# Performance work log

Hardware: AMD Instinct MI355X
Metric: run time of the kernel (lower is better)

## Reference

```python
import jax, jax.numpy as jnp
import numpy as np

L, B, S, H, NH, HD = 2, 2, 1024, 768, 12, 64
E, K, F, V = 8, 2, 3072, 50257
THETA = 10000.0
EPS = 1e-5


def setup_inputs() -> dict:
    key = jax.random.key(0)
    ks = iter(jax.random.split(key, 40))
    def nrm(shape):
        return jax.random.normal(next(ks), shape, jnp.float32) * 0.02
    return {
        "input_ids": jax.random.randint(next(ks), (B, S), 0, V),
        "emb": nrm((V, H)),
        "ln1_w": jnp.ones((L, H)), "ln1_b": jnp.zeros((L, H)),
        "ln2_w": jnp.ones((L, H)), "ln2_b": jnp.zeros((L, H)),
        "lnf_w": jnp.ones((H,)), "lnf_b": jnp.zeros((H,)),
        "Wq": nrm((L, H, H)), "bq": jnp.zeros((L, H)),
        "Wk": nrm((L, H, H)), "bk": jnp.zeros((L, H)),
        "Wv": nrm((L, H, H)), "bv": jnp.zeros((L, H)),
        "Wo": nrm((L, H, H)), "bo": jnp.zeros((L, H)),
        "Wr": nrm((L, H, E)), "br": jnp.zeros((L, E)),
        "W1": nrm((L, E, H, F)), "b1": jnp.zeros((L, E, F)),
        "W2": nrm((L, E, F, H)), "b2": jnp.zeros((L, E, H)),
    }


def _layer_norm(x, w, b):
    m = x.mean(-1, keepdims=True)
    v = ((x - m) ** 2).mean(-1, keepdims=True)
    return (x - m) * jax.lax.rsqrt(v + EPS) * w + b


def _rotate_half(x):
    x1, x2 = jnp.split(x, 2, axis=-1)
    return jnp.concatenate([-x2, x1], axis=-1)


def _forward(input_ids, emb, ln1_w, ln1_b, ln2_w, ln2_b, lnf_w, lnf_b,
             Wq, bq, Wk, bk, Wv, bv, Wo, bo, Wr, br, W1, b1, W2, b2):
    x = emb[input_ids]  # [B,S,H]

    # RoPE tables [1,1,S,HD]
    inv_freq = 1.0 / (THETA ** (jnp.arange(0, HD, 2, dtype=jnp.float32) / HD))
    freqs = jnp.arange(S, dtype=jnp.float32)[:, None] * inv_freq[None, :]
    ang = jnp.concatenate([freqs, freqs], axis=-1)
    cos = jnp.cos(ang)[None, None].astype(x.dtype)
    sin = jnp.sin(ang)[None, None].astype(x.dtype)

    causal = jnp.where(jnp.tril(jnp.ones((S, S), dtype=bool)), 0.0, -1e9)
    causal = causal[None, None].astype(x.dtype)

    scale = 1.0 / np.sqrt(HD)
    for l in range(L):
        # --- attention block ---
        h = _layer_norm(x, ln1_w[l], ln1_b[l])
        q = (h @ Wq[l] + bq[l]).reshape(B, S, NH, HD).transpose(0, 2, 1, 3)
        k = (h @ Wk[l] + bk[l]).reshape(B, S, NH, HD).transpose(0, 2, 1, 3)
        v = (h @ Wv[l] + bv[l]).reshape(B, S, NH, HD).transpose(0, 2, 1, 3)
        q = q * cos + _rotate_half(q) * sin
        k = k * cos + _rotate_half(k) * sin
        scores = jnp.einsum('bhqd,bhkd->bhqk', q, k) * scale + causal
        attn = jax.nn.softmax(scores, axis=-1)
        o = jnp.einsum('bhqk,bhkd->bhqd', attn, v)
        o = o.transpose(0, 2, 1, 3).reshape(B, S, H)
        x = x + (o @ Wo[l] + bo[l])

        # --- MoE feed-forward block ---
        h = _layer_norm(x, ln2_w[l], ln2_b[l]).reshape(-1, H)  # [N,H]
        router_probs = jax.nn.softmax(h @ Wr[l] + br[l], axis=-1)  # [N,E]
        tp, ti = jax.lax.top_k(router_probs, K)
        tp = tp / (tp.sum(-1, keepdims=True) + 1e-9)
        # combine weights per expert (equiv. to the per-slot scatter loop)
        w = (jax.nn.one_hot(ti, E, dtype=h.dtype) * tp[..., None]).sum(1)  # [N,E]
        a = jax.nn.gelu(jnp.einsum('nh,ehf->nef', h, W1[l]) + b1[l], approximate=False)
        oe = jnp.einsum('nef,efh->neh', a, W2[l]) + b2[l]
        ff = jnp.einsum('ne,neh->nh', w, oe)
        x = x + ff.reshape(B, S, H)

    x = _layer_norm(x, lnf_w, lnf_b)
    logits = jnp.einsum('bsh,vh->bsv', x, emb)  # tied lm_head
    return logits


def reference(input_ids, emb, ln1_w, ln1_b, ln2_w, ln2_b, lnf_w, lnf_b,
              Wq, bq, Wk, bk, Wv, bv, Wo, bo, Wr, br, W1, b1, W2, b2):
    return _forward(input_ids, emb, ln1_w, ln1_b, ln2_w, ln2_b, lnf_w, lnf_b,
                    Wq, bq, Wk, bk, Wv, bv, Wo, bo, Wr, br, W1, b1, W2, b2)
```

## Files before the change

kernel.cpp:

```cpp
#include <hip/hip_runtime.h>
#include <stdint.h>

constexpr int L = 2, Bb = 2, S = 1024, H = 768, NHd = 12, HD = 64;
constexpr int E = 8, F = 3072, V = 50257;
constexpr int NTOK = Bb * S;
constexpr int NSLOT = NTOK * 2;
constexpr float EPSLN = 1e-5f;

typedef __attribute__((ext_vector_type(4))) float f32x4;
typedef __attribute__((ext_vector_type(8))) short s16x8;

#define DEVI __device__ __forceinline__

DEVI float bf2f(short u) {
  union { float f; uint32_t i; } c; c.i = ((uint32_t)(uint16_t)u) << 16; return c.f;
}
DEVI short f2bf(float f) {
  union { float f; uint32_t i; } c; c.f = f;
  uint32_t x = c.i;
  uint32_t r = (x + 0x7fffu + ((x >> 16) & 1u)) >> 16;
  return (short)r;
}

DEVI void gload16(const void* g, void* l) {
  __builtin_amdgcn_global_load_lds(g, l, 16, 0, 0);
}

DEVI float gelu1(float g) { return 0.5f * g * (1.f + erff(g * 0.70710678118f)); }

__global__ void k_f32_to_bf16(const float* __restrict__ in, short* __restrict__ out, long n4) {
  long i = (long)blockIdx.x * blockDim.x + threadIdx.x;
  if (i >= n4) return;
  long base = i * 4;
  f32x4 v = *(const f32x4*)(in + base);
  short4 o;
  o.x = f2bf(v.x); o.y = f2bf(v.y); o.z = f2bf(v.z); o.w = f2bf(v.w);
  *(short4*)(out + base) = o;
}

__global__ void k_split(const float* __restrict__ in, short* __restrict__ oh,
                        short* __restrict__ ol, long n4) {
  long i = (long)blockIdx.x * blockDim.x + threadIdx.x;
  if (i >= n4) return;
  long base = i * 4;
  f32x4 v = *(const f32x4*)(in + base);
  short4 h, l;
  h.x = f2bf(v.x); l.x = f2bf(v.x - bf2f(h.x));
  h.y = f2bf(v.y); l.y = f2bf(v.y - bf2f(h.y));
  h.z = f2bf(v.z); l.z = f2bf(v.z - bf2f(h.z));
  h.w = f2bf(v.w); l.w = f2bf(v.w - bf2f(h.w));
  *(short4*)(oh + base) = h;
  *(short4*)(ol + base) = l;
}

__global__ void k_split3(const float* __restrict__ in, short* __restrict__ o0,
                         short* __restrict__ o1, short* __restrict__ o2, long n4) {
  long i = (long)blockIdx.x * blockDim.x + threadIdx.x;
  if (i >= n4) return;
  long base = i * 4;
  f32x4 v = *(const f32x4*)(in + base);
  short4 a, b, c;
#define SP3(comp)                                    \
  {                                                  \
    float x = v.comp;                                \
    short t0 = f2bf(x);                              \
    float r = x - bf2f(t0);                          \
    short t1 = f2bf(r);                              \
    short t2 = f2bf(r - bf2f(t1));                   \
    a.comp = t0; b.comp = t1; c.comp = t2;           \
  }
  SP3(x) SP3(y) SP3(z) SP3(w)
#undef SP3
  *(short4*)(o0 + base) = a;
  *(short4*)(o1 + base) = b;
  *(short4*)(o2 + base) = c;
}

__global__ void k_transpose_bf16(const float* __restrict__ in, short* __restrict__ out,
                                 int R, int C, long inBS, long outBS) {
  __shared__ float tile[32][33];
  const float* src = in + (size_t)blockIdx.z * inBS;
  short* dst = out + (size_t)blockIdx.z * outBS;
  int r0 = blockIdx.y * 32, c0 = blockIdx.x * 32;
  int tx = threadIdx.x, ty = threadIdx.y;
#pragma unroll
  for (int i = 0; i < 32; i += 8) {
    int r = r0 + ty + i, c = c0 + tx;
    if (r < R && c < C) tile[ty + i][tx] = src[(size_t)r * C + c];
  }
  __syncthreads();
#pragma unroll
  for (int i = 0; i < 32; i += 8) {
    int c = c0 + ty + i, r = r0 + tx;
    if (r < R && c < C) dst[(size_t)c * R + r] = f2bf(tile[tx][ty + i]);
  }
}

__global__ void k_transpose_split(const float* __restrict__ in, short* __restrict__ oh,
                                  short* __restrict__ ol, int R, int C, long inBS,
                                  long outBS) {
  __shared__ float tile[32][33];
  const float* src = in + (size_t)blockIdx.z * inBS;
  short* dh = oh + (size_t)blockIdx.z * outBS;
  short* dl = ol + (size_t)blockIdx.z * outBS;
  int r0 = blockIdx.y * 32, c0 = blockIdx.x * 32;
  int tx = threadIdx.x, ty = threadIdx.y;
#pragma unroll
  for (int i = 0; i < 32; i += 8) {
// ... 12 lines not shown
      dl[(size_t)c * R + r] = lo;
    }
  }
}

__global__ void k_transpose_split3(const float* __restrict__ in, short* __restrict__ o0,
                                   short* __restrict__ o1, short* __restrict__ o2,
                                   int R, int C) {
  __shared__ float tile[32][33];
  int r0 = blockIdx.y * 32, c0 = blockIdx.x * 32;
  int tx = threadIdx.x, ty = threadIdx.y;
#pragma unroll
  for (int i = 0; i < 32; i += 8) {
    int r = r0 + ty + i, c = c0 + tx;
    if (r < R && c < C) tile[ty + i][tx] = in[(size_t)r * C + c];
  }
  __syncthreads();
#pragma unroll
  for (int i = 0; i < 32; i += 8) {
    int c = c0 + ty + i, r = r0 + tx;
    if (r < R && c < C) {
      float v = tile[tx][ty + i];
      short t0 = f2bf(v);
      float rr = v - bf2f(t0);
      short t1 = f2bf(rr);
      short t2 = f2bf(rr - bf2f(t1));
      o0[(size_t)c * R + r] = t0;
      o1[(size_t)c * R + r] = t1;
      o2[(size_t)c * R + r] = t2;
    }
  }
}

__global__ void k_bqkv(const float* __restrict__ bq, const float* __restrict__ bk,
                       const float* __restrict__ bv, float* __restrict__ bqkv) {
  int i = blockIdx.x * blockDim.x + threadIdx.x;
  if (i >= L * 3 * H) return;
  int l = i / (3 * H), j = i % (3 * H);
  float v = (j < H) ? bq[l * H + j] : (j < 2 * H) ? bk[l * H + j - H] : bv[l * H + j - 2 * H];
  bqkv[i] = v;
}

__global__ void k_ropetab(float* __restrict__ cosT, float* __restrict__ sinT) {
  int i = blockIdx.x * blockDim.x + threadIdx.x;
  if (i >= S * (HD / 2)) return;
  int s = i / 32, d = i % 32;
  float invf = powf(10000.f, -(2.f * d) / (float)HD);
  float ang = (float)s * invf;
  cosT[i] = cosf(ang);
  sinT[i] = sinf(ang);
}

__global__ void k_embed(const int* __restrict__ ids, const float* __restrict__ emb,
                        float* __restrict__ x) {
  int idx = blockIdx.x * blockDim.x + threadIdx.x;
  int row = idx / (H / 4), c4 = idx % (H / 4);
  if (row >= NTOK) return;
  int t = ids[row];
  ((f32x4*)(x + (size_t)row * H))[c4] = ((const f32x4*)(emb + (size_t)t * H))[c4];
}

template <bool BF>
__global__ void k_layernorm(const float* __restrict__ x, const float* __restrict__ w,
                            const float* __restrict__ b, void* __restrict__ outp) {
  int row = blockIdx.x * (blockDim.x >> 6) + (threadIdx.x >> 6);
  int lane = threadIdx.x & 63;
  if (row >= NTOK) return;
  const float* xr = x + (size_t)row * H;
  float v[12], s = 0.f, s2 = 0.f;
#pragma unroll
  for (int j = 0; j < 12; j++) { float t = xr[lane + j * 64]; v[j] = t; s += t; s2 += t * t; }
#pragma unroll
  for (int off = 32; off; off >>= 1) { s += __shfl_xor(s, off); s2 += __shfl_xor(s2, off); }
  float m = s / (float)H;
  float var = s2 / (float)H - m * m;
  float rs = 1.f / sqrtf(var + EPSLN);
#pragma unroll
  for (int j = 0; j < 12; j++) {
    int c = lane + j * 64;
    float val = (v[j] - m) * rs * w[c] + b[c];
    if (BF) ((short*)outp)[(size_t)row * H + c] = f2bf(val);
    else    ((float*)outp)[(size_t)row * H + c] = val;
  }
}

__global__ void k_rope(const float* __restrict__ qkv, const float* __restrict__ bqkv,
                       const float* __restrict__ cosT, const float* __restrict__ sinT,
                       float* __restrict__ qf, float* __restrict__ kf,
                       float* __restrict__ vT) {
  int idx = blockIdx.x * blockDim.x + threadIdx.x;
  if (idx >= Bb * S * NHd * 32) return;
  int d = idx & 31;
  int h = (idx >> 5) % NHd;
  int t = idx / (32 * NHd);
  int s = t % S, b = t / S;
  const float* base = qkv + (size_t)t * (3 * H) + h * HD;
  const float* bb = bqkv + h * HD;
  float c = cosT[s * 32 + d], sn = sinT[s * 32 + d];
  float q1 = base[d] + bb[d],               q2 = base[d + 32] + bb[d + 32];
  float k1 = base[H + d] + bb[H + d],       k2 = base[H + d + 32] + bb[H + d + 32];
  float v1 = base[2 * H + d] + bb[2 * H + d], v2 = base[2 * H + d + 32] + bb[2 * H + d + 32];
  size_t z = (size_t)(b * NHd + h);
  size_t qk = (z * S + s) * HD;
  qf[qk + d]      = q1 * c - q2 * sn;
  qf[qk + d + 32] = q2 * c + q1 * sn;
  kf[qk + d]      = k1 * c - k2 * sn;
  kf[qk + d + 32] = k2 * c + k1 * sn;
  size_t vb = z * HD * S + s;
  vT[vb + (size_t)d * S]        = v1;
  vT[vb + (size_t)(d + 32) * S] = v2;
}

__global__ void k_softmax2(short* __restrict__ p0, short* __restrict__ p1) {
  int row = blockIdx.x * 4 + (threadIdx.x >> 6);
  int lane = threadIdx.x & 63;
  s16x8* r0 = (s16x8*)(p0 + (size_t)row * S + lane * 16);
  s16x8* r1 = (s16x8*)(p1 + (size_t)row * S + lane * 16);
  s16x8 h0 = r0[0], h1 = r0[1];
  s16x8 l0 = r1[0], l1 = r1[1];
  float v[16];
#pragma unroll
  for (int j = 0; j < 8; j++) {
    v[j] = bf2f(h0[j]) + bf2f(l0[j]);
    v[8 + j] = bf2f(h1[j]) + bf2f(l1[j]);
  }
  float mx = -3e38f;
#pragma unroll
  for (int j = 0; j < 16; j++) mx = fmaxf(mx, v[j]);
#pragma unroll
  for (int off = 32; off; off >>= 1) mx = fmaxf(mx, __shfl_xor(mx, off));
  float sum = 0.f;
#pragma unroll
  for (int j = 0; j < 16; j++) { v[j] = expf(v[j] - mx); sum += v[j]; }
#pragma unroll
  for (int off = 32; off; off >>= 1) sum += __shfl_xor(sum, off);
  float inv = 1.f / sum;
#pragma unroll
  for (int j = 0; j < 16; j++) v[j] *= inv;
  s16x8 oh0, oh1, ol0, ol1;
#pragma unroll
  for (int j = 0; j < 8; j++) {
    short hi = f2bf(v[j]);
    oh0[j] = hi; ol0[j] = f2bf(v[j] - bf2f(hi));
// ... 63 lines not shown
  if (tok >= NTOK) return;
  for (int k = 0; k < 2; k++) {
    int e = sel_e[tok * 2 + k];
    int pos = atomicAdd(cursor + e, 1);
    int g = offs[e] + pos;
    tok_list[g] = tok;
    slot_of[tok * 2 + k] = g;
  }
}

__global__ void k_combine(const float* __restrict__ oe, const float* __restrict__ sel_w,
                          const int* __restrict__ slot_of, const int* __restrict__ sel_e,
                          const float* __restrict__ b2, float* __restrict__ x) {
  int idx = blockIdx.x * blockDim.x + threadIdx.x;
  if (idx >= NTOK * (H / 4)) return;
  int tok = idx / (H / 4), c4 = idx % (H / 4);
  float w0 = sel_w[tok * 2], w1 = sel_w[tok * 2 + 1];
  int s0 = slot_of[tok * 2], s1 = slot_of[tok * 2 + 1];
  int e0 = sel_e[tok * 2], e1 = sel_e[tok * 2 + 1];
  f32x4 a = ((const f32x4*)(oe + (size_t)s0 * H))[c4];
  f32x4 b = ((const f32x4*)(oe + (size_t)s1 * H))[c4];
  f32x4 ba = ((const f32x4*)(b2 + (size_t)e0 * H))[c4];
  f32x4 bb = ((const f32x4*)(b2 + (size_t)e1 * H))[c4];
  f32x4* xp = (f32x4*)(x + (size_t)tok * H) + c4;
  *xp = *xp + w0 * (a + ba) + w1 * (b + bb);
}

template <int SP, int MODE, bool GATHER>
__global__ __launch_bounds__(256, 2) void k_bgemmS(
    const short* __restrict__ A0, const short* __restrict__ A1, const short* __restrict__ A2,
    long sAz, int lda,
    const short* __restrict__ B0, const short* __restrict__ B1, const short* __restrict__ B2,
    long sBz, int ldb,
    void* __restrict__ Cp, void* __restrict__ Cp2, int zdiv, long sChi, long sClo, int ldc,
    const float* __restrict__ res, const float* __restrict__ bias, long sBias,
    int M, int N, int K,
    const int* __restrict__ d_counts, const int* __restrict__ d_offs,
    const int* __restrict__ gidx, float alpha) {
  const int z = blockIdx.z;
  const int Meff = d_counts ? d_counts[z] : M;
  const int tm = blockIdx.y;
  if (tm * 128 >= Meff) return;
  const int tn = blockIdx.x;
  const int row_base = d_offs ? d_offs[z] : 0;

  __shared__ short Ab[SP][128 * 32];
  __shared__ short Bb2[SP][128 * 32];

  const int tid = threadIdx.x;
  const int lane = tid & 63;
  const int w = tid >> 6;

  const short* APz[3];
  const short* BPz[3];
  APz[0] = A0 + (size_t)z * sAz;
  APz[1] = A1 + (size_t)z * sAz;
  APz[2] = (SP > 2) ? (A2 + (size_t)z * sAz) : APz[0];
  BPz[0] = B0 + (size_t)z * sBz;
  BPz[1] = B1 + (size_t)z * sBz;
  BPz[2] = (SP > 2) ? (B2 + (size_t)z * sBz) : BPz[0];

  size_t aOff[2], bOff[2];
#pragma unroll
  for (int i = 0; i < 2; ++i) {
    const int srow = i * 64 + (tid >> 2);
    const int kb = (tid & 3) ^ (srow & 3);
    int lrow = tm * 128 + srow;
// ... 27 lines not shown
  for (int k0 = 0; k0 < K; k0 += 32) {
#pragma unroll
    for (int s = 0; s < SP; ++s) {
      gload16(APz[s] + aOff[0], (char*)(&Ab[s][0]) + w * 1024);
      gload16(APz[s] + aOff[1], (char*)(&Ab[s][0]) + 4096 + w * 1024);
      gload16(BPz[s] + bOff[0], (char*)(&Bb2[s][0]) + w * 1024);
      gload16(BPz[s] + bOff[1], (char*)(&Bb2[s][0]) + 4096 + w * 1024);
    }
    aOff[0] += 32; aOff[1] += 32; bOff[0] += 32; bOff[1] += 32;
    __syncthreads();
    s16x8 af[SP][4], bf[SP][4];
#pragma unroll
    for (int s = 0; s < SP; ++s)
#pragma unroll
      for (int i = 0; i < 4; ++i) {
        af[s][i] = *(const s16x8*)(&Ab[s][aoff[i]]);
        bf[s][i] = *(const s16x8*)(&Bb2[s][boff[i]]);
      }
#pragma unroll
    for (int mi = 0; mi < 4; ++mi)
#pragma unroll
      for (int ni = 0; ni < 4; ++ni) {
        f32x4 a = acc[mi][ni];
#pragma unroll
        for (int si = 0; si < SP; ++si)
#pragma unroll
          for (int sj = 0; sj < SP - si; ++sj)
            a = __builtin_amdgcn_mfma_f32_16x16x32_bf16(af[si][mi], bf[sj][ni], a, 0, 0, 0);
        acc[mi][ni] = a;
      }
    __syncthreads();
  }

  const long out_off = (long)(z / zdiv) * sChi + (long)(z % zdiv) * sClo;
  const float* bz = bias ? (bias + (size_t)z * sBias) : nullptr;
  const int q4 = lane >> 4;
  float bvv[4];
  int gco[4];
#pragma unroll
  for (int ni = 0; ni < 4; ++ni) {
    gco[ni] = tn * 128 + wc + ni * 16 + r16;
    bvv[ni] = (bz && gco[ni] < N) ? bz[gco[ni]] : 0.f;
  }
#pragma unroll
  for (int mi = 0; mi < 4; ++mi) {
#pragma unroll
    for (int j = 0; j < 4; ++j) {
      const int lrow = tm * 128 + wr + mi * 16 + q4 * 4 + j;
      if (lrow >= Meff) continue;
      const long rbase = out_off + (long)(row_base + lrow) * ldc;
#pragma unroll
      for (int ni = 0; ni < 4; ++ni) {
        if (gco[ni] >= N) continue;
        const float v = acc[mi][ni][j];
        const long idx = rbase + gco[ni];
        if (MODE == 0) {
          ((float*)Cp)[idx] = v + bvv[ni];
        } else if (MODE == 1) {
          ((float*)Cp)[idx] = res[idx] + v + bvv[ni];
        } else if (MODE == 6) {
          float g = gelu1(v + bvv[ni]);
          short hi = f2bf(g);
          ((short*)Cp)[idx] = hi;
          ((short*)Cp2)[idx] = f2bf(g - bf2f(hi));
        } else if (MODE == 7) {
          float g = v * alpha + ((gco[ni] > lrow) ? -1e9f : 0.f);
          short hi = f2bf(g);
          ((short*)Cp)[idx] = hi;
          ((short*)Cp2)[idx] = f2bf(g - bf2f(hi));
        }
      }
    }
  }
}

template <int SP, int MODE, bool GATHER>
static void bgemmS(hipStream_t st, const short* A0, const short* A1, const short* A2, long sAz,
                   int lda, const short* B0, const short* B1, const short* B2, long sBz,
                   int ldb, void* C, void* C2, int zdiv, long sChi, long sClo, int ldc,
                   const float* res, const float* bias, long sBias, int M, int N, int K,
                   int nz, const int* cnts, const int* offs_, const int* gat, float alpha) {
  dim3 g((N + 127) / 128, (M + 127) / 128, nz);
  k_bgemmS<SP, MODE, GATHER><<<g, 256, 0, st>>>(A0, A1, A2, sAz, lda, B0, B1, B2, sBz, ldb, C,
                                                C2, zdiv, sChi, sClo, ldc, res, bias, sBias, M,
                                                N, K, cnts, offs_, gat, alpha);
}

template <int MODE, bool GATHER, bool NSWZ>
__global__ __launch_bounds__(256, 2) void k_bgemm(
    const short* __restrict__ A, long sAz, int lda,
    const short* __restrict__ Bt, long sBz, int ldb,
    void* __restrict__ Cp, int zdiv, long sChi, long sClo, int ldc,
    const float* __restrict__ bias, long sBias,
    int M, int N, int K,
    const int* __restrict__ d_counts, const int* __restrict__ d_offs,
    const int* __restrict__ gidx) {
  const int z = blockIdx.z;
  const int Meff = d_counts ? d_counts[z] : M;
  int tm, tn;
  if (NSWZ) {
    const int bid = blockIdx.y * gridDim.x + blockIdx.x;
    const int nwg = gridDim.x * gridDim.y;
    const int q = nwg >> 3, r = nwg & 7;
    const int xcd = bid & 7, ix = bid >> 3;
    const int wg = (xcd < r) ? (xcd * (q + 1) + ix) : (r * (q + 1) + (xcd - r) * q + ix);
    tn = wg / gridDim.y;
    tm = wg % gridDim.y;
  } else {
    tm = blockIdx.y;
    tn = blockIdx.x;
  }
  if (tm * 128 >= Meff) return;
  const int row_base = d_offs ? d_offs[z] : 0;

  __shared__ short Abuf[128 * 32];
  __shared__ short Bbuf[128 * 32];

  const int tid = threadIdx.x;
  const int lane = tid & 63;
  const int w = tid >> 6;

  const short* Az = A + (size_t)z * sAz;
  const short* Bz = Bt + (size_t)z * sBz;

  const short* aSrc[2];
  const short* bSrc[2];
#pragma unroll
  for (int i = 0; i < 2; ++i) {
    const int srow = i * 64 + (tid >> 2);
    const int kb = (tid & 3) ^ (srow & 3);
    int lrow = tm * 128 + srow;
    if (lrow > Meff - 1) lrow = Meff - 1;
    int ar = row_base + lrow;
    if (GATHER) ar = gidx[ar];
    aSrc[i] = Az + (size_t)ar * lda + kb * 8;
    int bcol = tn * 128 + srow;
    if (bcol > N - 1) bcol = N - 1;
    bSrc[i] = Bz + (size_t)bcol * ldb + kb * 8;
  }

  f32x4 acc[4][4];
#pragma unroll
  for (int a = 0; a < 4; ++a)
#pragma unroll
    for (int b = 0; b < 4; ++b) acc[a][b] = {0.f, 0.f, 0.f, 0.f};

  const int wr = (w >> 1) * 64;
  const int wc = (w & 1) * 64;
  const int r16 = lane & 15;
  const int kb4 = lane >> 4;
  const int swz = (kb4 ^ (r16 & 3)) * 8;
  int aoff[4], boff[4];
#pragma unroll
  for (int i = 0; i < 4; ++i) {
    aoff[i] = (wr + i * 16 + r16) * 32 + swz;
    boff[i] = (wc + i * 16 + r16) * 32 + swz;
  }
  char* const ldsA0 = (char*)Abuf + w * 1024;
  char* const ldsA1 = (char*)Abuf + 4096 + w * 1024;
  char* const ldsB0 = (char*)Bbuf + w * 1024;
  char* const ldsB1 = (char*)Bbuf + 4096 + w * 1024;

  for (int k0 = 0; k0 < K; k0 += 32) {
    gload16(aSrc[0], ldsA0);
    gload16(aSrc[1], ldsA1);
    gload16(bSrc[0], ldsB0);
    gload16(bSrc[1], ldsB1);
    aSrc[0] += 32; aSrc[1] += 32; bSrc[0] += 32; bSrc[1] += 32;
    __syncthreads();
    s16x8 af[4], bf[4];
#pragma unroll
    for (int i = 0; i < 4; ++i) {
      af[i] = *(const s16x8*)(Abuf + aoff[i]);
      bf[i] = *(const s16x8*)(Bbuf + boff[i]);
    }
#pragma unroll
    for (int mi = 0; mi < 4; ++mi)
#pragma unroll
      for (int ni = 0; ni < 4; ++ni)
        acc[mi][ni] =
            __builtin_amdgcn_mfma_f32_16x16x32_bf16(af[mi], bf[ni], acc[mi][ni], 0, 0, 0);
    __syncthreads();
  }

  const long out_off = (long)(z / zdiv) * sChi + (long)(z % zdiv) * sClo;
  const float* bz = bias ? (bias + (size_t)z * sBias) : nullptr;
  const int q4 = lane >> 4;
  float bvv[4];
  int gco[4];
#pragma unroll
  for (int ni = 0; ni < 4; ++ni) {
    gco[ni] = tn * 128 + wc + ni * 16 + r16;
    bvv[ni] = (bz && gco[ni] < N) ? bz[gco[ni]] : 0.f;
  }
#pragma unroll
  for (int mi = 0; mi < 4; ++mi) {
#pragma unroll
    for (int j = 0; j < 4; ++j) {
      const int lrow = tm * 128 + wr + mi * 16 + q4 * 4 + j;
      if (lrow >= Meff) continue;
      const long rbase = out_off + (row_base + lrow) * (long)ldc;
#pragma unroll
      for (int ni = 0; ni < 4; ++ni) {
        if (gco[ni] >= N) continue;
        const float v = acc[mi][ni][j];
        if (MODE == 0) {
          ((float*)Cp)[rbase + gco[ni]] = v + bvv[ni];
        } else if (MODE == 4) {
          float g = v + bvv[ni];
          ((short*)Cp)[rbase + gco[ni]] = f2bf(gelu1(g));
        }
      }
    }
  }
// ... 30 lines not shown
  const float* Wo = (const float*)d_in[14];
  const float* bo = (const float*)d_in[15];
  const float* Wr = (const float*)d_in[16];
  const float* br = (const float*)d_in[17];
  const float* W1 = (const float*)d_in[18];
  const float* b1 = (const float*)d_in[19];
  const float* W2 = (const float*)d_in[20];
  const float* b2 = (const float*)d_in[21];
  float* out = (float*)d_out;

  char* p = (char*)d_ws;
  auto alloc = [&](size_t bytes) {
    char* r = p;
    p += (bytes + 255) & ~(size_t)255;
    return r;
  };
  short* embB = (short*)alloc((size_t)V * H * 2);
  char* big = alloc((size_t)Bb * NHd * S * S * 2 * 2);
  short* p0   = (short*)big;
  short* p1   = p0 + (size_t)Bb * NHd * S * S;
  short* R_hi = (short*)big;
  short* R_lo = R_hi + (size_t)E * F * H;
  short* Wb0 = (short*)alloc((size_t)3 * H * H * 2);
  short* Wb1 = (short*)alloc((size_t)3 * H * H * 2);
  short* Wb2 = (short*)alloc((size_t)3 * H * H * 2);
  short* Wo0 = (short*)alloc((size_t)H * H * 2);
  short* Wo1 = (short*)alloc((size_t)H * H * 2);
  short* Wo2 = (short*)alloc((size_t)H * H * 2);
  float* bqkv = (float*)alloc((size_t)L * 3 * H * 4);
  float* cosT = (float*)alloc((size_t)S * 32 * 4);
  float* sinT = (float*)alloc((size_t)S * 32 * 4);
  float* x    = (float*)alloc((size_t)NTOK * H * 4);
  float* hbuf = (float*)alloc((size_t)NTOK * H * 4);
  float* qf   = (float*)alloc((size_t)NTOK * H * 4);
  float* kf   = (float*)alloc((size_t)NTOK * H * 4);
  float* vT   = (float*)alloc((size_t)NTOK * H * 4);
  float* o    = (float*)alloc((size_t)NTOK * H * 4);
  short* xb   = (short*)alloc((size_t)NTOK * H * 2);
  short* xb2  = (short*)alloc((size_t)NTOK * H * 2);
  short* h_hi = (short*)alloc((size_t)NTOK * H * 2);
  short* h_lo = (short*)alloc((size_t)NTOK * H * 2);
  short* h30  = (short*)alloc((size_t)NTOK * H * 2);
  short* h31  = (short*)alloc((size_t)NTOK * H * 2);
  short* h32  = (short*)alloc((size_t)NTOK * H * 2);
  short* q30  = (short*)alloc((size_t)NTOK * H * 2);
  short* q31  = (short*)alloc((size_t)NTOK * H * 2);
  short* q32  = (short*)alloc((size_t)NTOK * H * 2);
  short* k30  = (short*)alloc((size_t)NTOK * H * 2);
  short* k31  = (short*)alloc((size_t)NTOK * H * 2);
  short* k32  = (short*)alloc((size_t)NTOK * H * 2);
  short* v20  = (short*)alloc((size_t)NTOK * H * 2);
  short* v21  = (short*)alloc((size_t)NTOK * H * 2);
  short* o30  = (short*)alloc((size_t)NTOK * H * 2);
  short* o31  = (short*)alloc((size_t)NTOK * H * 2);
  short* o32  = (short*)alloc((size_t)NTOK * H * 2);
  char* uni = alloc((size_t)NSLOT * F * 4 + (size_t)NSLOT * H * 4);
  float* qkvl   = (float*)uni;
  short* act_hi = (short*)uni;
  short* act_lo = (short*)(uni + (size_t)NSLOT * F * 2);
  short* act_b  = (short*)uni;
  float* oe     = (float*)(uni + (size_t)NSLOT * F * 4);
  int* counts  = (int*)alloc(2 * E * 4);
  int* cursor  = counts + E;
  int* offs    = (int*)alloc((E + 1) * 4);
  int* sel_e   = (int*)alloc((size_t)NTOK * 2 * 4);
  float* sel_w = (float*)alloc((size_t)NTOK * 2 * 4);
  int* slot_of = (int*)alloc((size_t)NTOK * 2 * 4);
  int* tok_lst = (int*)alloc((size_t)NSLOT * 4);

  long nEmb4 = (long)V * H / 4;
  k_f32_to_bf16<<<(nEmb4 + 255) / 256, 256, 0, stream>>>(emb, embB, nEmb4);
  k_bqkv<<<(L * 3 * H + 255) / 256, 256, 0, stream>>>(bq, bk, bv, bqkv);
  k_ropetab<<<(S * 32 + 255) / 256, 256, 0, stream>>>(cosT, sinT);
  k_embed<<<(NTOK * (H / 4) + 255) / 256, 256, 0, stream>>>(ids, emb, x);

  dim3 tb(32, 8);
  const dim3 tHH(H / 32, H / 32, 1);
  const long n4tok = (long)NTOK * H / 4;
  const int nb4 = (NTOK * (H / 4) + 255) / 256;

  for (int l = 0; l < L; l++) {
    k_layernorm<false><<<NTOK / 4, 256, 0, stream>>>(x, ln1w + l * H, ln1b + l * H, hbuf);
    k_split3<<<(n4tok + 255) / 256, 256, 0, stream>>>(hbuf, h30, h31, h32, n4tok);
    k_transpose_split3<<<tHH, tb, 0, stream>>>(Wq + (size_t)l * H * H, Wb0, Wb1, Wb2, H, H);
    k_transpose_split3<<<tHH, tb, 0, stream>>>(Wk + (size_t)l * H * H, Wb0 + H * H,
                                               Wb1 + H * H, Wb2 + H * H, H, H);
    k_transpose_split3<<<tHH, tb, 0, stream>>>(Wv + (size_t)l * H * H, Wb0 + 2 * H * H,
                                               Wb1 + 2 * H * H, Wb2 + 2 * H * H, H, H);
    bgemmS<3, 0, false>(stream, h30, h31, h32, 0, H, Wb0, Wb1, Wb2, 0, H, qkvl, nullptr, 1, 0,
                        0, 3 * H, nullptr, nullptr, 0, NTOK, 3 * H, H, 1, nullptr, nullptr,
                        nullptr, 1.f);
    k_rope<<<(Bb * S * NHd * 32 + 255) / 256, 256, 0, stream>>>(qkvl, bqkv + l * 3 * H, cosT,
                                                                sinT, qf, kf, vT);
    k_split3<<<(n4tok + 255) / 256, 256, 0, stream>>>(qf, q30, q31, q32, n4tok);
    k_split3<<<(n4tok + 255) / 256, 256, 0, stream>>>(kf, k30, k31, k32, n4tok);
    k_split<<<(n4tok + 255) / 256, 256, 0, stream>>>(vT, v20, v21, n4tok);
    bgemmS<3, 7, false>(stream, q30, q31, q32, (long)S * HD, HD, k30, k31, k32, (long)S * HD,
                        HD, p0, p1, 1, (long)S * S, 0, S, nullptr, nullptr, 0, S, S, HD,
                        Bb * NHd, nullptr, nullptr, nullptr, 0.125f);
    k_softmax2<<<(Bb * NHd * S) / 4, 256, 0, stream>>>(p0, p1);
    bgemmS<2, 0, false>(stream, p0, p1, nullptr, (long)S * S, S, v20, v21, nullptr,
                        (long)HD * S, S, o, nullptr, NHd, (long)S * H, HD, H, nullptr, nullptr,
                        0, S, HD, S, Bb * NHd, nullptr, nullptr, nullptr, 1.f);
    k_split3<<<(n4tok + 255) / 256, 256, 0, stream>>>(o, o30, o31, o32, n4tok);
    k_transpose_split3<<<tHH, tb, 0, stream>>>(Wo + (size_t)l * H * H, Wo0, Wo1, Wo2, H, H);
    bgemmS<3, 1, false>(stream, o30, o31, o32, 0, H, Wo0, Wo1, Wo2, 0, H, x, nullptr, 1, 0, 0,
                        H, x, bo + l * H, 0, NTOK, H, H, 1, nullptr, nullptr, nullptr, 1.f);

    k_layernorm<false><<<NTOK / 4, 256, 0, stream>>>(x, ln2w + l * H, ln2b + l * H, hbuf);
    hipMemsetAsync(counts, 0, 2 * E * sizeof(int), stream);
    k_router<<<NTOK / 4, 256, 0, stream>>>(hbuf, Wr + (size_t)l * H * E, br + l * E, sel_w,
                                           sel_e, counts);
    k_offsets<<<1, 64, 0, stream>>>(counts, offs);
    k_scatter<<<(NTOK + 255) / 256, 256, 0, stream>>>(sel_e, offs, cursor, tok_lst, slot_of);
    if (l == 0) {
      k_split<<<(n4tok + 255) / 256, 256, 0, stream>>>(hbuf, h_hi, h_lo, n4tok);
      k_transpose_split<<<dim3(F / 32, H / 32, E), tb, 0, stream>>>(
          W1, R_hi, R_lo, H, F, (long)H * F, (long)F * H);
      bgemmS<2, 6, true>(stream, h_hi, h_lo, nullptr, 0, H, R_hi, R_lo, nullptr, (long)F * H,
                         H, act_hi, act_lo, 1, 0, 0, F, nullptr, b1, F, NSLOT, F, H, E, counts,
                         offs, tok_lst, 1.f);
      k_transpose_split<<<dim3(H / 32, F / 32, E), tb, 0, stream>>>(
          W2, R_hi, R_lo, F, H, (long)F * H, (long)H * F);
      bgemmS<2, 0, false>(stream, act_hi, act_lo, nullptr, 0, F, R_hi, R_lo, nullptr,
                          (long)H * F, F, oe, nullptr, 1, 0, 0, H, nullptr, nullptr, 0, NSLOT,
                          H, F, E, counts, offs, nullptr, 1.f);
      k_combine<<<nb4, 256, 0, stream>>>(oe, sel_w, slot_of, sel_e, b2, x);
    } else {
      k_transpose_bf16<<<dim3(F / 32, H / 32, E), tb, 0, stream>>>(
          W1 + (size_t)1 * E * H * F, R_hi, H, F, (long)H * F, (long)F * H);
      k_transpose_bf16<<<dim3(H / 32, F / 32, E), tb, 0, stream>>>(
          W2 + (size_t)1 * E * F * H, R_lo, F, H, (long)F * H, (long)H * F);
      k_f32_to_bf16<<<(n4tok + 255) / 256, 256, 0, stream>>>(hbuf, xb2, n4tok);
      bgemm<4, true, false>(stream, xb2, 0, H, R_hi, (long)F * H, H, act_b, 1, 0, 0, F,
                            b1 + (size_t)l * E * F, F, NSLOT, F, H, E, counts, offs, tok_lst);
      bgemm<0, false, false>(stream, act_b, 0, F, R_lo, (long)H * F, F, oe, 1, 0, 0, H,
                             nullptr, 0, NSLOT, H, F, E, counts, offs, nullptr);
      k_combine<<<nb4, 256, 0, stream>>>(oe, sel_w, slot_of, sel_e, b2 + (size_t)l * E * H, x);
    }
  }

  k_layernorm<true><<<NTOK / 4, 256, 0, stream>>>(x, lnfw, lnfb, xb);
  bgemm<0, false, true>(stream, xb, 0, H, embB, 0, H, out, 1, 0, 0, V, nullptr, 0, NTOK, V, H,
                        1, nullptr, nullptr, nullptr);
}
```

Baseline: 1.792 ms.

## Fuse bf16 splitting and RoPE into layernorm and GEMM epilogues; widen bgemm K tile

The bf16 hi/lo/lo2 splitting is now done inside the layernorm kernels and inside the GEMM epilogues instead of in separate split kernels. A new QKV epilogue mode applies bias, RoPE and the V transpose directly from the accumulators. The three weight transposes are merged into one launch. This removes several elementwise passes and their fp32 intermediate buffers. Separately, the plain bf16 GEMM now loads a 64-wide K step per iteration with a new LDS swizzle, which halves the barriers per K step but doubles LDS use. The cost is more register pressure and scattered stores in the GEMM epilogues.

```diff
diff --git a/kernel.cpp b/kernel.cpp
--- a/kernel.cpp
+++ b/kernel.cpp
@@ -36,44 +36,6 @@
   short4 o;
   o.x = f2bf(v.x); o.y = f2bf(v.y); o.z = f2bf(v.z); o.w = f2bf(v.w);
   *(short4*)(out + base) = o;
-}
-
-__global__ void k_split(const float* __restrict__ in, short* __restrict__ oh,
-                        short* __restrict__ ol, long n4) {
-  long i = (long)blockIdx.x * blockDim.x + threadIdx.x;
-  if (i >= n4) return;
-  long base = i * 4;
-  f32x4 v = *(const f32x4*)(in + base);
-  short4 h, l;
-  h.x = f2bf(v.x); l.x = f2bf(v.x - bf2f(h.x));
-  h.y = f2bf(v.y); l.y = f2bf(v.y - bf2f(h.y));
-  h.z = f2bf(v.z); l.z = f2bf(v.z - bf2f(h.z));
-  h.w = f2bf(v.w); l.w = f2bf(v.w - bf2f(h.w));
-  *(short4*)(oh + base) = h;
-  *(short4*)(ol + base) = l;
-}
-
-__global__ void k_split3(const float* __restrict__ in, short* __restrict__ o0,
-                         short* __restrict__ o1, short* __restrict__ o2, long n4) {
-  long i = (long)blockIdx.x * blockDim.x + threadIdx.x;
-  if (i >= n4) return;
-  long base = i * 4;
-  f32x4 v = *(const f32x4*)(in + base);
-  short4 a, b, c;
-#define SP3(comp)                                    \
-  {                                                  \
-    float x = v.comp;                                \
-    short t0 = f2bf(x);                              \
-    float r = x - bf2f(t0);                          \
-    short t1 = f2bf(r);                              \
-    short t2 = f2bf(r - bf2f(t1));                   \
-    a.comp = t0; b.comp = t1; c.comp = t2;           \
-  }
-  SP3(x) SP3(y) SP3(z) SP3(w)
-#undef SP3
-  *(short4*)(o0 + base) = a;
-  *(short4*)(o1 + base) = b;
-  *(short4*)(o2 + base) = c;
 }
 
 __global__ void k_transpose_bf16(const float* __restrict__ in, short* __restrict__ out,
@@ -152,6 +114,35 @@
   }
 }
 
+__global__ void k_wqkv_t3(const float* __restrict__ Wq, const float* __restrict__ Wk,
+                          const float* __restrict__ Wv, short* __restrict__ o0,
+                          short* __restrict__ o1, short* __restrict__ o2) {
+  __shared__ float tile[32][33];
+  const int zz = blockIdx.z;
+  const float* in = (zz == 0) ? Wq : (zz == 1) ? Wk : Wv;
+  const size_t doff = (size_t)zz * H * H;
+  int r0 = blockIdx.y * 32, c0 = blockIdx.x * 32;
+  int tx = threadIdx.x, ty = threadIdx.y;
+#pragma unroll
+  for (int i = 0; i < 32; i += 8) {
+    int r = r0 + ty + i, c = c0 + tx;
+    tile[ty + i][tx] = in[(size_t)r * H + c];
+  }
+  __syncthreads();
+#pragma unroll
+  for (int i = 0; i < 32; i += 8) {
+    int c = c0 + ty + i, r = r0 + tx;
+    float v = tile[tx][ty + i];
+    short t0 = f2bf(v);
+    float rr = v - bf2f(t0);
+    short t1 = f2bf(rr);
+    short t2 = f2bf(rr - bf2f(t1));
+    o0[doff + (size_t)c * H + r] = t0;
+    o1[doff + (size_t)c * H + r] = t1;
+    o2[doff + (size_t)c * H + r] = t2;
+  }
+}
+
 __global__ void k_bqkv(const float* __restrict__ bq, const float* __restrict__ bk,
                        const float* __restrict__ bv, float* __restrict__ bqkv) {
   int i = blockIdx.x * blockDim.x + threadIdx.x;
@@ -180,55 +171,45 @@
   ((f32x4*)(x + (size_t)row * H))[c4] = ((const f32x4*)(emb + (size_t)t * H))[c4];
 }
 
-template <bool BF>
+template <int OUT>
 __global__ void k_layernorm(const float* __restrict__ x, const float* __restrict__ w,
-                            const float* __restrict__ b, void* __restrict__ outp) {
+                            const float* __restrict__ b, float* __restrict__ of,
+                            short* __restrict__ s0, short* __restrict__ s1,
+                            short* __restrict__ s2) {
   int row = blockIdx.x * (blockDim.x >> 6) + (threadIdx.x >> 6);
   int lane = threadIdx.x & 63;
   if (row >= NTOK) return;
   const float* xr = x + (size_t)row * H;
-  float v[12], s = 0.f, s2 = 0.f;
-#pragma unroll
-  for (int j = 0; j < 12; j++) { float t = xr[lane + j * 64]; v[j] = t; s += t; s2 += t * t; }
-#pragma unroll
-  for (int off = 32; off; off >>= 1) { s += __shfl_xor(s, off); s2 += __shfl_xor(s2, off); }
+  float v[12], s = 0.f, s2s = 0.f;
+#pragma unroll
+  for (int j = 0; j < 12; j++) { float t = xr[lane + j * 64]; v[j] = t; s += t; s2s += t * t; }
+#pragma unroll
+  for (int off = 32; off; off >>= 1) { s += __shfl_xor(s, off); s2s += __shfl_xor(s2s, off); }
   float m = s / (float)H;
-  float var = s2 / (float)H - m * m;
+  float var = s2s / (float)H - m * m;
   float rs = 1.f / sqrtf(var + EPSLN);
 #pragma unroll
   for (int j = 0; j < 12; j++) {
     int c = lane + j * 64;
     float val = (v[j] - m) * rs * w[c] + b[c];
-    if (BF) ((short*)outp)[(size_t)row * H + c] = f2bf(val);
-    else    ((float*)outp)[(size_t)row * H + c] = val;
-  }
-}
-
-__global__ void k_rope(const float* __restrict__ qkv, const float* __restrict__ bqkv,
-                       const float* __restrict__ cosT, const float* __restrict__ sinT,
-                       float* __restrict__ qf, float* __restrict__ kf,
-                       float* __restrict__ vT) {
-  int idx = blockIdx.x * blockDim.x + threadIdx.x;
-  if (idx >= Bb * S * NHd * 32) return;
-  int d = idx & 31;
-  int h = (idx >> 5) % NHd;
-  int t = idx / (32 * NHd);
-  int s = t % S, b = t / S;
-  const float* base = qkv + (size_t)t * (3 * H) + h * HD;
-  const float* bb = bqkv + h * HD;
-  float c = cosT[s * 32 + d], sn = sinT[s * 32 + d];
-  float q1 = base[d] + bb[d],               q2 = base[d + 32] + bb[d + 32];
-  float k1 = base[H + d] + bb[H + d],       k2 = base[H + d + 32] + bb[H + d + 32];
-  float v1 = base[2 * H + d] + bb[2 * H + d], v2 = base[2 * H + d + 32] + bb[2 * H + d + 32];
-  size_t z = (size_t)(b * NHd + h);
-  size_t qk = (z * S + s) * HD;
-  qf[qk + d]      = q1 * c - q2 * sn;
-  qf[qk + d + 32] = q2 * c + q1 * sn;
-  kf[qk + d]      = k1 * c - k2 * sn;
-  kf[qk + d + 32] = k2 * c + k1 * sn;
-  size_t vb = z * HD * S + s;
-  vT[vb + (size_t)d * S]        = v1;
-  vT[vb + (size_t)(d + 32) * S] = v2;
+    size_t idx = (size_t)row * H + c;
+    if (OUT == 1) {
+      short t0 = f2bf(val);
+      float rr = val - bf2f(t0);
+      short t1 = f2bf(rr);
+      short t2 = f2bf(rr - bf2f(t1));
+      s0[idx] = t0; s1[idx] = t1; s2[idx] = t2;
+    } else if (OUT == 2) {
+      of[idx] = val;
+      short hi = f2bf(val);
+      s0[idx] = hi; s1[idx] = f2bf(val - bf2f(hi));
+    } else if (OUT == 3) {
+      of[idx] = val;
+      s0[idx] = f2bf(val);
+    } else {
+      s0[idx] = f2bf(val);
+    }
+  }
 }
 
 __global__ void k_softmax2(short* __restrict__ p0, short* __restrict__ p1) {
@@ -358,7 +339,11 @@
     long sAz, int lda,
     const short* __restrict__ B0, const short* __restrict__ B1, const short* __restrict__ B2,
     long sBz, int ldb,
-    void* __restrict__ Cp, void* __restrict__ Cp2, int zdiv, long sChi, long sClo, int ldc,
+    void* __restrict__ Cp, void* __restrict__ Cp2, void* __restrict__ Cp3,
+    short* __restrict__ K0, short* __restrict__ K1, short* __restrict__ K2,
+    short* __restrict__ V0, short* __restrict__ V1,
+    const float* __restrict__ cT, const float* __restrict__ sT,
+    int zdiv, long sChi, long sClo, int ldc,
     const float* __restrict__ res, const float* __restrict__ bias, long sBias,
     int M, int N, int K,
     const int* __restrict__ d_counts, const int* __restrict__ d_offs,
@@ -452,7 +437,6 @@
     __syncthreads();
   }
 
-  const long out_off = (long)(z / zdiv) * sChi + (long)(z % zdiv) * sClo;
   const float* bz = bias ? (bias + (size_t)z * sBias) : nullptr;
   const int q4 = lane >> 4;
   float bvv[4];
@@ -462,6 +446,52 @@
     gco[ni] = tn * 128 + wc + ni * 16 + r16;
     bvv[ni] = (bz && gco[ni] < N) ? bz[gco[ni]] : 0.f;
   }
+
+  if (MODE == 9) {
+    const int sec_base = tn * 128 + wc;
+    const int sec = sec_base / H;
+    const int hh = (sec_base % H) / HD;
+#pragma unroll
+    for (int mi = 0; mi < 4; ++mi) {
+#pragma unroll
+      for (int j = 0; j < 4; ++j) {
+        const int row = tm * 128 + wr + mi * 16 + q4 * 4 + j;
+        const int ss = row & (S - 1);
+        const long zz = (long)((row >> 10) * NHd + hh);
+#pragma unroll
+        for (int ni = 0; ni < 2; ++ni) {
+          const int d = ni * 16 + r16;
+          float a1 = acc[mi][ni][j] + bvv[ni];
+          float a2 = acc[mi][ni + 2][j] + bvv[ni + 2];
+          if (sec < 2) {
+            float cc = cT[ss * 32 + d], sn = sT[ss * 32 + d];
+            float r1 = a1 * cc - a2 * sn;
+            float r2 = a2 * cc + a1 * sn;
+            const long bi = (zz * S + ss) * HD + d;
+            short* d0 = (sec == 0) ? (short*)Cp : K0;
+            short* d1 = (sec == 0) ? (short*)Cp2 : K1;
+            short* d2 = (sec == 0) ? (short*)Cp3 : K2;
+            short t0 = f2bf(r1); float rr = r1 - bf2f(t0);
+            short t1 = f2bf(rr); short t2 = f2bf(rr - bf2f(t1));
+            d0[bi] = t0; d1[bi] = t1; d2[bi] = t2;
+            t0 = f2bf(r2); rr = r2 - bf2f(t0);
+            t1 = f2bf(rr); t2 = f2bf(rr - bf2f(t1));
+            d0[bi + 32] = t0; d1[bi + 32] = t1; d2[bi + 32] = t2;
+          } else {
+            const long vb1 = zz * HD * S + (long)d * S + ss;
+            short hv = f2bf(a1);
+            V0[vb1] = hv; V1[vb1] = f2bf(a1 - bf2f(hv));
+            const long vb2 = vb1 + 32L * S;
+            hv = f2bf(a2);
+            V0[vb2] = hv; V1[vb2] = f2bf(a2 - bf2f(hv));
+          }
+        }
+      }
+    }
+    return;
+  }
+
+  const long out_off = (long)(z / zdiv) * sChi + (long)(z % zdiv) * sClo;
 #pragma unroll
   for (int mi = 0; mi < 4; ++mi) {
 #pragma unroll
@@ -488,6 +518,13 @@
           short hi = f2bf(g);
           ((short*)Cp)[idx] = hi;
           ((short*)Cp2)[idx] = f2bf(g - bf2f(hi));
+        } else if (MODE == 8) {
+          float g = v + bvv[ni];
+          short t0 = f2bf(g); float rr = g - bf2f(t0);
+          short t1 = f2bf(rr); short t2 = f2bf(rr - bf2f(t1));
+          ((short*)Cp)[idx] = t0;
+          ((short*)Cp2)[idx] = t1;
+          ((short*)Cp3)[idx] = t2;
         }
       }
     }
@@ -497,13 +534,17 @@
 template <int SP, int MODE, bool GATHER>
 static void bgemmS(hipStream_t st, const short* A0, const short* A1, const short* A2, long sAz,
                    int lda, const short* B0, const short* B1, const short* B2, long sBz,
-                   int ldb, void* C, void* C2, int zdiv, long sChi, long sClo, int ldc,
-                   const float* res, const float* bias, long sBias, int M, int N, int K,
-                   int nz, const int* cnts, const int* offs_, const int* gat, float alpha) {
+                   int ldb, void* C, void* C2, void* C3, int zdiv, long sChi, long sClo,
+                   int ldc, const float* res, const float* bias, long sBias, int M, int N,
+                   int K, int nz, const int* cnts, const int* offs_, const int* gat,
+                   float alpha, short* K0 = nullptr, short* K1 = nullptr, short* K2 = nullptr,
+                   short* V0 = nullptr, short* V1 = nullptr, const float* cT = nullptr,
+                   const float* sT = nullptr) {
   dim3 g((N + 127) / 128, (M + 127) / 128, nz);
   k_bgemmS<SP, MODE, GATHER><<<g, 256, 0, st>>>(A0, A1, A2, sAz, lda, B0, B1, B2, sBz, ldb, C,
-                                                C2, zdiv, sChi, sClo, ldc, res, bias, sBias, M,
-                                                N, K, cnts, offs_, gat, alpha);
+                                                C2, C3, K0, K1, K2, V0, V1, cT, sT, zdiv, sChi,
+                                                sClo, ldc, res, bias, sBias, M, N, K, cnts,
+                                                offs_, gat, alpha);
 }
 
 template <int MODE, bool GATHER, bool NSWZ>
@@ -533,8 +574,8 @@
   if (tm * 128 >= Meff) return;
   const int row_base = d_offs ? d_offs[z] : 0;
 
-  __shared__ short Abuf[128 * 32];
-  __shared__ short Bbuf[128 * 32];
+  __shared__ short Abuf[128 * 64];
+  __shared__ short Bbuf[128 * 64];
 
   const int tid = threadIdx.x;
   const int lane = tid & 63;
@@ -543,20 +584,20 @@
   const short* Az = A + (size_t)z * sAz;
   const short* Bz = Bt + (size_t)z * sBz;
 
-  const short* aSrc[2];
-  const short* bSrc[2];
-#pragma unroll
-  for (int i = 0; i < 2; ++i) {
-    const int srow = i * 64 + (tid >> 2);
-    const int kb = (tid & 3) ^ (srow & 3);
-    int lrow = tm * 128 + srow;
+  const int swzS = ((lane >> 3) ^ (lane & 7)) * 8;
+  const short* aSrc[4];
+  const short* bSrc[4];
+#pragma unroll
+  for (int i = 0; i < 4; ++i) {
+    const int rin = (w * 4 + i) * 8 + (lane >> 3);
+    int lrow = tm * 128 + rin;
     if (lrow > Meff - 1) lrow = Meff - 1;
     int ar = row_base + lrow;
     if (GATHER) ar = gidx[ar];
-    aSrc[i] = Az + (size_t)ar * lda + kb * 8;
-    int bcol = tn * 128 + srow;
+    aSrc[i] = Az + (size_t)ar * lda + swzS;
+    int bcol = tn * 128 + rin;
     if (bcol > N - 1) bcol = N - 1;
-    bSrc[i] = Bz + (size_t)bcol * ldb + kb * 8;
+    bSrc[i] = Bz + (size_t)bcol * ldb + swzS;
   }
 
   f32x4 acc[4][4];
@@ -569,37 +610,40 @@
   const int wc = (w & 1) * 64;
   const int r16 = lane & 15;
   const int kb4 = lane >> 4;
-  const int swz = (kb4 ^ (r16 & 3)) * 8;
-  int aoff[4], boff[4];
+  int aoff[4][2], boff[4][2];
 #pragma unroll
   for (int i = 0; i < 4; ++i) {
-    aoff[i] = (wr + i * 16 + r16) * 32 + swz;
-    boff[i] = (wc + i * 16 + r16) * 32 + swz;
-  }
-  char* const ldsA0 = (char*)Abuf + w * 1024;
-  char* const ldsA1 = (char*)Abuf + 4096 + w * 1024;
-  char* const ldsB0 = (char*)Bbuf + w * 1024;
-  char* const ldsB1 = (char*)Bbuf + 4096 + w * 1024;
-
-  for (int k0 = 0; k0 < K; k0 += 32) {
-    gload16(aSrc[0], ldsA0);
-    gload16(aSrc[1], ldsA1);
-    gload16(bSrc[0], ldsB0);
-    gload16(bSrc[1], ldsB1);
-    aSrc[0] += 32; aSrc[1] += 32; bSrc[0] += 32; bSrc[1] += 32;
+#pragma unroll
+    for (int kw = 0; kw < 2; ++kw) {
+      const int sw = ((r16 & 7) ^ (kw * 4 + kb4)) * 8;
+      aoff[i][kw] = (wr + i * 16 + r16) * 64 + sw;
+      boff[i][kw] = (wc + i * 16 + r16) * 64 + sw;
+    }
+  }
+
+  for (int k0 = 0; k0 < K; k0 += 64) {
+#pragma unroll
+    for (int i = 0; i < 4; ++i) gload16(aSrc[i], (char*)Abuf + (w * 4 + i) * 1024);
+#pragma unroll
+    for (int i = 0; i < 4; ++i) gload16(bSrc[i], (char*)Bbuf + (w * 4 + i) * 1024);
+#pragma unroll
+    for (int i = 0; i < 4; ++i) { aSrc[i] += 64; bSrc[i] += 64; }
     __syncthreads();
-    s16x8 af[4], bf[4];
-#pragma unroll
-    for (int i = 0; i < 4; ++i) {
-      af[i] = *(const s16x8*)(Abuf + aoff[i]);
-      bf[i] = *(const s16x8*)(Bbuf + boff[i]);
-    }
-#pragma unroll
-    for (int mi = 0; mi < 4; ++mi)
-#pragma unroll
-      for (int ni = 0; ni < 4; ++ni)
-        acc[mi][ni] =
-            __builtin_amdgcn_mfma_f32_16x16x32_bf16(af[mi], bf[ni], acc[mi][ni], 0, 0, 0);
+#pragma unroll
+    for (int kw = 0; kw < 2; ++kw) {
+      s16x8 af[4], bf[4];
+#pragma unroll
+      for (int i = 0; i < 4; ++i) {
+        af[i] = *(const s16x8*)(Abuf + aoff[i][kw]);
+        bf[i] = *(const s16x8*)(Bbuf + boff[i][kw]);
+      }
+#pragma unroll
+      for (int mi = 0; mi < 4; ++mi)
+#pragma unroll
+        for (int ni = 0; ni < 4; ++ni)
+          acc[mi][ni] =
+              __builtin_amdgcn_mfma_f32_16x16x32_bf16(af[mi], bf[ni], acc[mi][ni], 0, 0, 0);
+    }
     __syncthreads();
   }
 
@@ -696,10 +740,6 @@
   float* sinT = (float*)alloc((size_t)S * 32 * 4);
   float* x    = (float*)alloc((size_t)NTOK * H * 4);
   float* hbuf = (float*)alloc((size_t)NTOK * H * 4);
-  float* qf   = (float*)alloc((size_t)NTOK * H * 4);
-  float* kf   = (float*)alloc((size_t)NTOK * H * 4);
-  float* vT   = (float*)alloc((size_t)NTOK * H * 4);
-  float* o    = (float*)alloc((size_t)NTOK * H * 4);
   short* xb   = (short*)alloc((size_t)NTOK * H * 2);
   short* xb2  = (short*)alloc((size_t)NTOK * H * 2);
   short* h_hi = (short*)alloc((size_t)NTOK * H * 2);
@@ -719,7 +759,6 @@
   short* o31  = (short*)alloc((size_t)NTOK * H * 2);
   short* o32  = (short*)alloc((size_t)NTOK * H * 2);
   char* uni = alloc((size_t)NSLOT * F * 4 + (size_t)NSLOT * H * 4);
-  float* qkvl   = (float*)uni;
   short* act_hi = (short*)uni;
   short* act_lo = (short*)(uni + (size_t)NSLOT * F * 2);
   short* act_b  = (short*)uni;
@@ -740,71 +779,66 @@
 
   dim3 tb(32, 8);
   const dim3 tHH(H / 32, H / 32, 1);
-  const long n4tok = (long)NTOK * H / 4;
-  const int nb4 = (NTOK * (H / 4) + 255) / 256;
 
   for (int l = 0; l < L; l++) {
-    k_layernorm<false><<<NTOK / 4, 256, 0, stream>>>(x, ln1w + l * H, ln1b + l * H, hbuf);
-    k_split3<<<(n4tok + 255) / 256, 256, 0, stream>>>(hbuf, h30, h31, h32, n4tok);
-    k_transpose_split3<<<tHH, tb, 0, stream>>>(Wq + (size_t)l * H * H, Wb0, Wb1, Wb2, H, H);
-    k_transpose_split3<<<tHH, tb, 0, stream>>>(Wk + (size_t)l * H * H, Wb0 + H * H,
-                                               Wb1 + H * H, Wb2 + H * H, H, H);
-    k_transpose_split3<<<tHH, tb, 0, stream>>>(Wv + (size_t)l * H * H, Wb0 + 2 * H * H,
-                                               Wb1 + 2 * H * H, Wb2 + 2 * H * H, H, H);
-    bgemmS<3, 0, false>(stream, h30, h31, h32, 0, H, Wb0, Wb1, Wb2, 0, H, qkvl, nullptr, 1, 0,
-                        0, 3 * H, nullptr, nullptr, 0, NTOK, 3 * H, H, 1, nullptr, nullptr,
-                        nullptr, 1.f);
-    k_rope<<<(Bb * S * NHd * 32 + 255) / 256, 256, 0, stream>>>(qkvl, bqkv + l * 3 * H, cosT,
-                                                                sinT, qf, kf, vT);
-    k_split3<<<(n4tok + 255) / 256, 256, 0, stream>>>(qf, q30, q31, q32, n4tok);
-    k_split3<<<(n4tok + 255) / 256, 256, 0, stream>>>(kf, k30, k31, k32, n4tok);
-    k_split<<<(n4tok + 255) / 256, 256, 0, stream>>>(vT, v20, v21, n4tok);
+    k_layernorm<1><<<NTOK / 4, 256, 0, stream>>>(x, ln1w + l * H, ln1b + l * H, nullptr, h30,
+                                                 h31, h32);
+    k_wqkv_t3<<<dim3(H / 32, H / 32, 3), tb, 0, stream>>>(
+        Wq + (size_t)l * H * H, Wk + (size_t)l * H * H, Wv + (size_t)l * H * H, Wb0, Wb1, Wb2);
+    bgemmS<3, 9, false>(stream, h30, h31, h32, 0, H, Wb0, Wb1, Wb2, 0, H, q30, q31, q32, 1, 0,
+                        0, 0, nullptr, bqkv + l * 3 * H, 0, NTOK, 3 * H, H, 1, nullptr,
+                        nullptr, nullptr, 1.f, k30, k31, k32, v20, v21, cosT, sinT);
     bgemmS<3, 7, false>(stream, q30, q31, q32, (long)S * HD, HD, k30, k31, k32, (long)S * HD,
-                        HD, p0, p1, 1, (long)S * S, 0, S, nullptr, nullptr, 0, S, S, HD,
-                        Bb * NHd, nullptr, nullptr, nullptr, 0.125f);
+                        HD, p0, p1, nullptr, 1, (long)S * S, 0, S, nullptr, nullptr, 0, S, S,
+                        HD, Bb * NHd, nullptr, nullptr, nullptr, 0.125f);
     k_softmax2<<<(Bb * NHd * S) / 4, 256, 0, stream>>>(p0, p1);
-    bgemmS<2, 0, false>(stream, p0, p1, nullptr, (long)S * S, S, v20, v21, nullptr,
-                        (long)HD * S, S, o, nullptr, NHd, (long)S * H, HD, H, nullptr, nullptr,
-                        0, S, HD, S, Bb * NHd, nullptr, nullptr, nullptr, 1.f);
-    k_split3<<<(n4tok + 255) / 256, 256, 0, stream>>>(o, o30, o31, o32, n4tok);
+    bgemmS<2, 8, false>(stream, p0, p1, nullptr, (long)S * S, S, v20, v21, nullptr,
+                        (long)HD * S, S, o30, o31, o32, NHd, (long)S * H, HD, H, nullptr,
+                        nullptr, 0, S, HD, S, Bb * NHd, nullptr, nullptr, nullptr, 1.f);
     k_transpose_split3<<<tHH, tb, 0, stream>>>(Wo + (size_t)l * H * H, Wo0, Wo1, Wo2, H, H);
-    bgemmS<3, 1, false>(stream, o30, o31, o32, 0, H, Wo0, Wo1, Wo2, 0, H, x, nullptr, 1, 0, 0,
-                        H, x, bo + l * H, 0, NTOK, H, H, 1, nullptr, nullptr, nullptr, 1.f);
-
-    k_layernorm<false><<<NTOK / 4, 256, 0, stream>>>(x, ln2w + l * H, ln2b + l * H, hbuf);
+    bgemmS<3, 1, false>(stream, o30, o31, o32, 0, H, Wo0, Wo1, Wo2, 0, H, x, nullptr, nullptr,
+                        1, 0, 0, H, x, bo + l * H, 0, NTOK, H, H, 1, nullptr, nullptr, nullptr,
+                        1.f);
+
+    if (l == 0)
+      k_layernorm<2><<<NTOK / 4, 256, 0, stream>>>(x, ln2w + l * H, ln2b + l * H, hbuf, h_hi,
+                                                   h_lo, nullptr);
+    else
+      k_layernorm<3><<<NTOK / 4, 256, 0, stream>>>(x, ln2w + l * H, ln2b + l * H, hbuf, xb2,
+                                                   nullptr, nullptr);
     hipMemsetAsync(counts, 0, 2 * E * sizeof(int), stream);
     k_router<<<NTOK / 4, 256, 0, stream>>>(hbuf, Wr + (size_t)l * H * E, br + l * E, sel_w,
                                            sel_e, counts);
     k_offsets<<<1, 64, 0, stream>>>(counts, offs);
     k_scatter<<<(NTOK + 255) / 256, 256, 0, stream>>>(sel_e, offs, cursor, tok_lst, slot_of);
     if (l == 0) {
-      k_split<<<(n4tok + 255) / 256, 256, 0, stream>>>(hbuf, h_hi, h_lo, n4tok);
       k_transpose_split<<<dim3(F / 32, H / 32, E), tb, 0, stream>>>(
           W1, R_hi, R_lo, H, F, (long)H * F, (long)F * H);
       bgemmS<2, 6, true>(stream, h_hi, h_lo, nullptr, 0, H, R_hi, R_lo, nullptr, (long)F * H,
-                         H, act_hi, act_lo, 1, 0, 0, F, nullptr, b1, F, NSLOT, F, H, E, counts,
-                         offs, tok_lst, 1.f);
+                         H, act_hi, act_lo, nullptr, 1, 0, 0, F, nullptr, b1, F, NSLOT, F, H,
+                         E, counts, offs, tok_lst, 1.f);
       k_transpose_split<<<dim3(H / 32, F / 32, E), tb, 0, stream>>>(
           W2, R_hi, R_lo, F, H, (long)F * H, (long)H * F);
       bgemmS<2, 0, false>(stream, act_hi, act_lo, nullptr, 0, F, R_hi, R_lo, nullptr,
-                          (long)H * F, F, oe, nullptr, 1, 0, 0, H, nullptr, nullptr, 0, NSLOT,
-                          H, F, E, counts, offs, nullptr, 1.f);
-      k_combine<<<nb4, 256, 0, stream>>>(oe, sel_w, slot_of, sel_e, b2, x);
+                          (long)H * F, F, oe, nullptr, nullptr, 1, 0, 0, H, nullptr, nullptr,
+                          0, NSLOT, H, F, E, counts, offs, nullptr, 1.f);
+      k_combine<<<(NTOK * (H / 4) + 255) / 256, 256, 0, stream>>>(oe, sel_w, slot_of, sel_e,
+                                                                  b2, x);
     } else {
       k_transpose_bf16<<<dim3(F / 32, H / 32, E), tb, 0, stream>>>(
           W1 + (size_t)1 * E * H * F, R_hi, H, F, (long)H * F, (long)F * H);
       k_transpose_bf16<<<dim3(H / 32, F / 32, E), tb, 0, stream>>>(
           W2 + (size_t)1 * E * F * H, R_lo, F, H, (long)F * H, (long)H * F);
-      k_f32_to_bf16<<<(n4tok + 255) / 256, 256, 0, stream>>>(hbuf, xb2, n4tok);
       bgemm<4, true, false>(stream, xb2, 0, H, R_hi, (long)F * H, H, act_b, 1, 0, 0, F,
                             b1 + (size_t)l * E * F, F, NSLOT, F, H, E, counts, offs, tok_lst);
       bgemm<0, false, false>(stream, act_b, 0, F, R_lo, (long)H * F, F, oe, 1, 0, 0, H,
                              nullptr, 0, NSLOT, H, F, E, counts, offs, nullptr);
-      k_combine<<<nb4, 256, 0, stream>>>(oe, sel_w, slot_of, sel_e, b2 + (size_t)l * E * H, x);
-    }
-  }
-
-  k_layernorm<true><<<NTOK / 4, 256, 0, stream>>>(x, lnfw, lnfb, xb);
+      k_combine<<<(NTOK * (H / 4) + 255) / 256, 256, 0, stream>>>(oe, sel_w, slot_of, sel_e,
+                                                                  b2 + (size_t)l * E * H, x);
+    }
+  }
+
+  k_layernorm<4><<<NTOK / 4, 256, 0, stream>>>(x, lnfw, lnfb, nullptr, xb, nullptr, nullptr);
   bgemm<0, false, true>(stream, xb, 0, H, embB, 0, H, out, 1, 0, 0, V, nullptr, 0, NTOK, V, H,
                         1, nullptr, nullptr, nullptr);
 }
```

After: 1.700 ms. 1.05x faster.
